# Optimization experiments

Measured on AMD Instinct MI355X. Metric: run time of the kernel, lower is better.

Reference implementation:

```python
import jax, jax.numpy as jnp
import numpy as np

IN_FEATURES = 256
WIDTH = 512
GRID_POINTS = 32   # num control points
DEGREE = 3         # spline_order
BATCH = 8192
LN_EPS = 1e-5


def make_knots(num_ctrl_pts, degree):
    knot_count = num_ctrl_pts + degree + 1
    knots = np.zeros(knot_count, dtype=np.float32)
    knots[-(degree + 1):] = 1.0
    interior = knot_count - 2 * (degree + 1)
    if interior > 0:
        knots[degree + 1:degree + 1 + interior] = np.linspace(0.0, 1.0, interior + 2, dtype=np.float32)[1:-1]
    return jnp.asarray(knots)

KNOTS = make_knots(GRID_POINTS, DEGREE)  # [num_ctrl + degree + 1]


def bspline_basis(x, knots, degree):
    # x: [b, f] in [0,1]; returns [b, f, num_ctrl_pts]
    xe = x[..., None]                      # [b, f, 1]
    left = knots[:-1]
    right = knots[1:]
    basis = ((xe >= left) & (xe < right)).astype(x.dtype)            # [b,f,K-1]
    last = ((xe >= left[-1]) & (xe <= right[-1])).astype(x.dtype)    # [b,f,1]
    basis = jnp.concatenate([basis[..., :-1], last], axis=-1)
    for r in range(1, degree + 1):  # fixed small loop over spline order
        m = basis.shape[-1] - 1
        if m <= 0:
            break
        idx = np.arange(m)
        lk = knots[idx]                 # [m]
        rk = knots[idx + r + 1]
        d1 = knots[idx + r] - knots[idx]
        d2 = knots[idx + r + 1] - knots[idx + 1]
        s1 = jnp.where(d1 > 0, d1, 1.0)  # safe denominators (avoid nan in both where branches)
        s2 = jnp.where(d2 > 0, d2, 1.0)
        t1 = jnp.where(d1 > 0, (xe - lk) / s1, 0.0) * basis[..., :m]
        t2 = jnp.where(d2 > 0, (rk - xe) / s2, 0.0) * basis[..., 1:m + 1]
        basis = t1 + t2
    return basis


def setup_inputs() -> dict:
    key = jax.random.key(0)
    ks = jax.random.split(key, 8)
    coeff_init = np.sqrt(2.0 / (GRID_POINTS * IN_FEATURES)).astype(np.float32)
    return {
        "inputs": jax.random.normal(ks[0], (BATCH, IN_FEATURES), dtype=jnp.float32),
        "input_shift": jnp.zeros((IN_FEATURES,), dtype=jnp.float32),
        "input_log_scale": jnp.zeros((IN_FEATURES,), dtype=jnp.float32),
        "spline_coeffs": coeff_init * jax.random.normal(ks[1], (IN_FEATURES, GRID_POINTS, WIDTH), dtype=jnp.float32),
        "bias": jnp.zeros((WIDTH,), dtype=jnp.float32),
        "skip_w": jax.random.normal(ks[2], (IN_FEATURES, WIDTH), dtype=jnp.float32) / np.sqrt(IN_FEATURES).astype(np.float32),
        "skip_b": jnp.zeros((WIDTH,), dtype=jnp.float32),
        "ln_gamma": jnp.ones((WIDTH,), dtype=jnp.float32),
        "ln_beta": jnp.zeros((WIDTH,), dtype=jnp.float32),
    }


def reference(inputs, input_shift, input_log_scale, spline_coeffs, bias,
              skip_w, skip_b, ln_gamma, ln_beta):
    scale = jax.nn.softplus(input_log_scale) + 0.001
    normalised = jax.nn.sigmoid((inputs - input_shift) * scale)            # [b,f] in (0,1)
    basis = bspline_basis(normalised, KNOTS, DEGREE)                       # [b,f,g]
    spline_mix = jnp.einsum('bfg,fgw->bw', basis, spline_coeffs)
    linear_skip = inputs @ skip_w + skip_b
    combined = spline_mix + linear_skip + bias
    mu = jnp.mean(combined, axis=-1, keepdims=True)
    var = jnp.mean(jnp.square(combined - mu), axis=-1, keepdims=True)
    normed = (combined - mu) * jax.lax.rsqrt(var + LN_EPS) * ln_gamma + ln_beta
    return jax.nn.gelu(normed, approximate=False)  # torch nn.GELU default = exact erf
```

## Files before the change

### kernel.cpp

```cpp
#include <hip/hip_runtime.h>
#include <hip/hip_bf16.h>
#include <math.h>

#define BATCH 8192
#define F 256
#define G 32
#define W 512
#define NCHUNK 132
#define NPER 66

typedef float f32x4 __attribute__((ext_vector_type(4)));
typedef short s16x8 __attribute__((ext_vector_type(8)));
typedef long long i64x2 __attribute__((ext_vector_type(2)));
typedef unsigned long long u64;

__device__ __forceinline__ short f2bf(float f) {
  unsigned int u = __builtin_bit_cast(unsigned int, f);
  u += 0x7fffu + ((u >> 16) & 1u);
  return (short)(u >> 16);
}

__device__ __forceinline__ float bf2f(unsigned short h) {
  unsigned int u = ((unsigned int)h) << 16;
  return __builtin_bit_cast(float, u);
}

__device__ __forceinline__ float knotv(int i) {
  int j = i - 3;
  j = j < 0 ? 0 : (j > 29 ? 29 : j);
  return (float)j * (1.0f / 29.0f);
}

__device__ __forceinline__ float fdiv_fast(float a, float b) {
  return a * __builtin_amdgcn_rcpf(b);
}

__global__ __launch_bounds__(256) void pre_build(
    const float* __restrict__ coeffs, const float* __restrict__ skip_w,
    const float* __restrict__ inp, const float* __restrict__ shift,
    const float* __restrict__ lscale,
    short* __restrict__ Bws, unsigned long long* __restrict__ nvq,
    unsigned char* __restrict__ s0q)
{
  __shared__ float T[64][17];
  __shared__ float sfc[16], sfh[16];
  const int tid = threadIdx.x;

  if (blockIdx.x < 2112) {
    const int gid = blockIdx.x * 256 + tid;
    const int lane = gid & 63;
    const int kk = (gid >> 6) & 1;
    const int nf = (gid >> 7) & 3;
    const int wn = (gid >> 9) & 1;
    const int nt = (gid >> 10) & 3;
    const int c  = gid >> 12;
    const int w  = nt * 128 + wn * 64 + nf * 16 + (lane & 15);
    const int kl = kk * 32 + (lane >> 4) * 8;
    const float* src = (c < 128) ? (coeffs + (size_t)(c * 64 + kl) * W + w)
                                 : (skip_w + (size_t)((c - 128) * 64 + kl) * W + w);
    s16x8 h;
    #pragma unroll
    for (int j = 0; j < 8; ++j) h[j] = f2bf(src[(size_t)j * W]);
    ((s16x8*)Bws)[gid] = h;
    return;
  }

  const int bb = blockIdx.x - 2112;
  const int b0 = (bb & 127) * 64;
  const int f0 = (bb >> 7) * 16;

  {
    const int r = tid >> 2, q = tid & 3;
    float4 v = *(const float4*)(inp + (size_t)(b0 + r) * F + f0 + q * 4);
    T[r][q * 4 + 0] = v.x;
    T[r][q * 4 + 1] = v.y;
    T[r][q * 4 + 2] = v.z;
    T[r][q * 4 + 3] = v.w;
  }
  if (tid < 16) {
    float ls = lscale[f0 + tid];
    sfc[tid] = fmaxf(ls, 0.0f) + __logf(1.0f + __expf(-fabsf(ls))) + 0.001f;
    sfh[tid] = shift[f0 + tid];
  }
  __syncthreads();

  const int lane = tid & 63;
  const int wid = tid >> 6;
  #pragma unroll
  for (int j = 0; j < 4; ++j) {
    const int fl = wid * 4 + j;
    const int f = f0 + fl;
    const float z = (T[lane][fl] - sfh[fl]) * sfc[fl];
    const float sg = 1.0f / (1.0f + __expf(-z));
    int s0 = (int)(sg * 29.0f);
    s0 = s0 < 0 ? 0 : (s0 > 28 ? 28 : s0);
    const int sp = s0 + 3;
    float Nv[4], lef[4], rig[4];
    Nv[0] = 1.0f;
    #pragma unroll
    for (int r = 1; r <= 3; ++r) {
      lef[r] = sg - knotv(sp + 1 - r);
      rig[r] = knotv(sp + r) - sg;
      float saved = 0.0f;
      #pragma unroll
      for (int jj = 0; jj < r; ++jj) {
        float temp = fdiv_fast(Nv[jj], rig[jj + 1] + lef[r - jj]);
        Nv[jj] = saved + rig[jj + 1] * temp;
        saved = lef[r - jj] * temp;
      }
      Nv[r] = saved;
    }
    const u64 nv =
        (u64)(unsigned short)f2bf(Nv[0])
      | ((u64)(unsigned short)f2bf(Nv[1]) << 16)
      | ((u64)(unsigned short)f2bf(Nv[2]) << 32)
      | ((u64)(unsigned short)f2bf(Nv[3]) << 48);
    nvq[(size_t)f * BATCH + b0 + lane] = nv;
    s0q[(size_t)f * BATCH + b0 + lane] = (unsigned char)s0;
  }
}

__device__ __forceinline__ void stage_nv(short* __restrict__ Ab, int cc,
    int stoff, int hi, int bp, int m0,
    unsigned long long nv, int s0, const float* __restrict__ inp)
{
  short* base = Ab + stoff;
  if (cc < 128) {
    const int pp = s0 & 7, ga = s0 >> 3;
    const int s = 16 * pp, shl = s & 63;
    const unsigned long long a = nv << shl;
    const unsigned long long b = (nv >> (63 - shl)) >> 1;
    const bool hs = (s >= 64);
    i64x2 d0, d1, z;
    d0[0] = hs ? 0ll : (long long)a;
    d0[1] = hs ? (long long)a : (long long)b;
    d1[0] = hs ? (long long)b : 0ll;
    d1[1] = 0ll;
    z[0] = 0ll; z[1] = 0ll;
    *(i64x2*)(base + ga * 128) = d0;
    *(i64x2*)(base + ((ga + 1) & 3) * 128) = d1;
    *(i64x2*)(base + ((ga + 2) & 3) * 128) = z;
    *(i64x2*)(base + ((ga + 3) & 3) * 128) = z;
  } else {
    const int sb = (cc - 128) * 64 + hi * 32;
    const float* ip = inp + (size_t)(m0 + bp) * F + sb;
    #pragma unroll
    for (int lq = 0; lq < 4; ++lq) {
      s16x8 h;
      #pragma unroll
      for (int j = 0; j < 8; ++j) h[j] = f2bf(ip[lq * 8 + j]);
      *(s16x8*)(base + lq * 128) = h;
    }
  }
}

__global__ __launch_bounds__(256, 2) void kan_gemm_v9(
    const float* __restrict__ inp, const short* __restrict__ Bws,
    const unsigned long long* __restrict__ nvq, const unsigned char* __restrict__ s0q,
    const float* __restrict__ bias, const float* __restrict__ skip_b,
    float* __restrict__ outf, short* __restrict__ Cws)
{
  __shared__ short Abuf[2][8192];

  const int tid = threadIdx.x;
  const int lane = tid & 63;
  const int wid = tid >> 6;
  const int kh = wid >> 1;
  const int nh = wid & 1;

  const int nb = ((blockIdx.x & 7) << 6) | (blockIdx.x >> 3);
  const int mt = nb >> 2, nt = nb & 3;
  const int m0 = mt * 64, n0 = nt * 128;

  const int ci = tid >> 7;
  const int hi = (tid >> 6) & 1;
  const int bp = tid & 63;
  const int mg = bp >> 4, l15b = bp & 15;
  const int stoff = ci * 4096 + ((mg * 2 + hi) * 64 + l15b) * 8;

  f32x4 acc[4][4];
  #pragma unroll
  for (int i = 0; i < 4; ++i)
    #pragma unroll
    for (int j = 0; j < 4; ++j)
      acc[i][j] = (f32x4){0.f, 0.f, 0.f, 0.f};

  const short* bq = Bws + (size_t)(((kh * 4 + nt) * 2 + nh) * 8) * 512 + lane * 8;

#define LOADB(BS) do {                                                          \
    _Pragma("unroll")                                                           \
    for (int nf = 0; nf < 4; ++nf)                                              \
      _Pragma("unroll")                                                         \
      for (int kk = 0; kk < 2; ++kk)                                            \
        BS[nf * 2 + kk] = *(const s16x8*)(bq + (nf * 2 + kk) * 512);            \
    bq += 65536;                                                                \
  } while (0)

#define PREF(NVL, S0L, PTGT) do {                                               \
    const int cc_ = 2 * (PTGT) + ci;                                            \
    if ((PTGT) < NPER && cc_ < 128) {                                           \
      const size_t ix_ = (size_t)(2 * cc_ + hi) * BATCH + m0 + bp;              \
      NVL = nvq[ix_];                                                           \
      S0L = (int)s0q[ix_];                                                      \
    }                                                                           \
  } while (0)

#define MMAC(AB, BS)                                                            \
    _Pragma("unroll")                                                           \
    for (int kk = 0; kk < 2; ++kk)                                              \
      _Pragma("unroll")                                                         \
      for (int mf = 0; mf < 4; ++mf) {                                          \
        s16x8 af = *(const s16x8*)&AB[kh * 4096 + ((mf * 2 + kk) * 64 + lane) * 8]; \
        _Pragma("unroll")                                                       \
        for (int nf = 0; nf < 4; ++nf)                                          \
          acc[mf][nf] = __builtin_amdgcn_mfma_f32_16x16x32_bf16(                \
              af, BS[nf * 2 + kk], acc[mf][nf], 0, 0, 0);                       \
      }

#define PERIOD(P_, ACUR, ANXT, BCUR, BNXT, NVU, S0U, NVL, S0L) do {             \
    asm volatile("s_waitcnt lgkmcnt(0)" ::: "memory");                          \
    __builtin_amdgcn_s_barrier();                                               \
    PREF(NVL, S0L, (P_) + 2);                                                   \
    if ((P_) + 1 < NPER) {                                                      \
      LOADB(BNXT);                                                              \
      stage_nv(ANXT, 2 * ((P_) + 1) + ci, stoff, hi, bp, m0, NVU, S0U, inp);    \
    }                                                                           \
    __builtin_amdgcn_s_setprio(1);                                              \
    MMAC(ACUR, BCUR);                                                           \
    __builtin_amdgcn_s_setprio(0);                                              \
  } while (0)

  s16x8 bA[8], bB[8];
  unsigned long long nvA = 0, nvB = 0;
  int s0A = 0, s0B = 0;

  PREF(nvA, s0A, 0);
  LOADB(bA);
  stage_nv(&Abuf[0][0], 2 * 0 + ci, stoff, hi, bp, m0, nvA, s0A, inp);
  PREF(nvB, s0B, 1);

  for (int p = 0; p < NPER; p += 2) {
    PERIOD(p,     (&Abuf[0][0]), (&Abuf[1][0]), bA, bB, nvB, s0B, nvA, s0A);
    PERIOD(p + 1, (&Abuf[1][0]), (&Abuf[0][0]), bB, bA, nvA, s0A, nvB, s0B);
  }
#undef PERIOD
#undef MMAC
#undef PREF
#undef LOADB

  __syncthreads();
  float* red = (float*)&Abuf[0][0];
  const int l15 = lane & 15;
  const int lq = lane >> 4;
  if (kh == 1) {
    #pragma unroll
    for (int mf = 0; mf < 4; ++mf)
      #pragma unroll
      for (int nf = 0; nf < 4; ++nf)
        *(f32x4*)&red[nh * 4096 + (mf * 4 + nf) * 256 + lane * 4] = acc[mf][nf];
  }
  __syncthreads();
  if (kh == 0) {
    #pragma unroll
    for (int nf = 0; nf < 4; ++nf) {
      const int col = n0 + nh * 64 + nf * 16 + l15;
      const float badd = bias[col] + skip_b[col];
      #pragma unroll
      for (int mf = 0; mf < 4; ++mf) {
        f32x4 part = *(const f32x4*)&red[nh * 4096 + (mf * 4 + nf) * 256 + lane * 4];
        const int r0 = m0 + mf * 16 + lq * 4;
        if (Cws) {
          #pragma unroll
          for (int r = 0; r < 4; ++r)
            Cws[(size_t)(r0 + r) * W + col] = f2bf(acc[mf][nf][r] + part[r] + badd);
        } else {
          #pragma unroll
          for (int r = 0; r < 4; ++r)
            outf[(size_t)(r0 + r) * W + col] = acc[mf][nf][r] + part[r] + badd;
        }
      }
    }
  }
}

__global__ __launch_bounds__(256, 1) void ln_gelu_bf(
    const short* __restrict__ Cws, float* __restrict__ out,
    const float* __restrict__ gamma, const float* __restrict__ beta)
{
  const int lane = threadIdx.x & 63;
  const int wid = threadIdx.x >> 6;
  const int row = blockIdx.x * 4 + wid;
  const short* p = Cws + (size_t)row * W + lane * 8;
  s16x8 hv = *(const s16x8*)p;
  float v[8];
  #pragma unroll
  for (int j = 0; j < 8; ++j) v[j] = bf2f((unsigned short)hv[j]);
  float s = 0.f, q = 0.f;
  #pragma unroll
  for (int j = 0; j < 8; ++j) { s += v[j]; q += v[j] * v[j]; }
  #pragma unroll
  for (int m = 1; m < 64; m <<= 1) {
    s += __shfl_xor(s, m);
    q += __shfl_xor(q, m);
  }
  const float mu = s * (1.0f / 512.0f);
  const float var = q * (1.0f / 512.0f) - mu * mu;
  const float inv = rsqrtf(var + 1e-5f);
  const float4 g0 = *(const float4*)(gamma + lane * 8);
  const float4 g1 = *(const float4*)(gamma + lane * 8 + 4);
  const float4 b0 = *(const float4*)(beta + lane * 8);
  const float4 b1 = *(const float4*)(beta + lane * 8 + 4);
  float gm[8] = {g0.x, g0.y, g0.z, g0.w, g1.x, g1.y, g1.z, g1.w};
  float bt[8] = {b0.x, b0.y, b0.z, b0.w, b1.x, b1.y, b1.z, b1.w};
  float o[8];
  #pragma unroll
  for (int j = 0; j < 8; ++j) {
    float x = (v[j] - mu) * inv * gm[j] + bt[j];
    o[j] = 0.5f * x * (1.0f + erff(x * 0.70710678f));
  }
  float* po = out + (size_t)row * W + lane * 8;
  float4 w0 = {o[0], o[1], o[2], o[3]};
  float4 w1 = {o[4], o[5], o[6], o[7]};
  *(float4*)po = w0;
  *(float4*)(po + 4) = w1;
}

__global__ __launch_bounds__(256, 1) void ln_gelu(
    float* __restrict__ out, const float* __restrict__ gamma,
    const float* __restrict__ beta)
{
  const int lane = threadIdx.x & 63;
  const int wid = threadIdx.x >> 6;
  const int row = blockIdx.x * 4 + wid;
  float* p = out + (size_t)row * W + lane * 8;
  float4 a = *(const float4*)p;
  float4 b = *(const float4*)(p + 4);
  float v[8] = {a.x, a.y, a.z, a.w, b.x, b.y, b.z, b.w};
  float s = 0.f, q = 0.f;
  #pragma unroll
  for (int j = 0; j < 8; ++j) { s += v[j]; q += v[j] * v[j]; }
  #pragma unroll
  for (int m = 1; m < 64; m <<= 1) {
    s += __shfl_xor(s, m);
    q += __shfl_xor(q, m);
  }
  const float mu = s * (1.0f / 512.0f);
  const float var = q * (1.0f / 512.0f) - mu * mu;
  const float inv = rsqrtf(var + 1e-5f);
  const float4 g0 = *(const float4*)(gamma + lane * 8);
  const float4 g1 = *(const float4*)(gamma + lane * 8 + 4);
  const float4 b0 = *(const float4*)(beta + lane * 8);
  const float4 b1 = *(const float4*)(beta + lane * 8 + 4);
  float gm[8] = {g0.x, g0.y, g0.z, g0.w, g1.x, g1.y, g1.z, g1.w};
  float bt[8] = {b0.x, b0.y, b0.z, b0.w, b1.x, b1.y, b1.z, b1.w};
  float o[8];
  #pragma unroll
  for (int j = 0; j < 8; ++j) {
    float x = (v[j] - mu) * inv * gm[j] + bt[j];
    o[j] = 0.5f * x * (1.0f + erff(x * 0.70710678f));
  }
  float4 w0 = {o[0], o[1], o[2], o[3]};
  float4 w1 = {o[4], o[5], o[6], o[7]};
  *(float4*)p = w0;
  *(float4*)(p + 4) = w1;
}

__device__ __forceinline__ void issue_b(int c, int uu, int n0,
                                        const float* __restrict__ coeffs,
                                        const float* __restrict__ skip_w,
                                        float (&r)[4][8]) {
  const float* base = (c < 128) ? (coeffs + (size_t)c * 64 * W)
                                : (skip_w + (size_t)(c - 128) * 64 * W);
  const int kk = (uu >> 6) & 1;
  const int lq = (uu >> 4) & 3;
  const int l15 = uu & 15;
  const int u7 = uu >> 7;
  #pragma unroll
  for (int s = 0; s < 4; ++s) {
    const int w = (2 * s + u7) * 16 + l15;
    const float* p = base + (size_t)(kk * 32 + lq * 8) * W + n0 + w;
    #pragma unroll
    for (int j = 0; j < 8; ++j) r[s][j] = p[(size_t)j * W];
  }
}

__global__ __launch_bounds__(512, 1) void kan_gemm_v2(
    const float* __restrict__ inp, const float* __restrict__ shift,
    const float* __restrict__ lscale, const float* __restrict__ coeffs,
    const float* __restrict__ bias, const float* __restrict__ skip_w,
    const float* __restrict__ skip_b, float* __restrict__ out)
{
  __shared__ short Abuf[2][8192];
  __shared__ short Bbuf[2][8192];
  __shared__ unsigned short sgl[F * 128];

  const int tid = threadIdx.x;
  const int lane = tid & 63;
  const int wid = tid >> 6;
  const int nb = (blockIdx.x & 7) * 32 + (blockIdx.x >> 3);
  const int mt = nb >> 2;
  const int nt = nb & 3;
  const int m0 = mt * 128;
  const int n0 = nt * 128;

  float bpref[4][8];
  if (tid >= 256) issue_b(0, tid - 256, n0, coeffs, skip_w, bpref);

  float* shf = (float*)&Abuf[0][0];
  if (tid < 256) {
    float ls = lscale[tid];
    shf[tid] = fmaxf(ls, 0.0f) + __logf(1.0f + __expf(-fabsf(ls))) + 0.001f;
    shf[256 + tid] = shift[tid];
  }
  __syncthreads();

  {
    const int row = tid & 127;
    const int q = tid >> 7;
    const float* ip = inp + (size_t)(m0 + row) * F + q * 64;
    #pragma unroll
    for (int i = 0; i < 16; ++i) {
      float4 v = *(const float4*)(ip + i * 4);
      float vv[4] = {v.x, v.y, v.z, v.w};
      #pragma unroll
      for (int j = 0; j < 4; ++j) {
        const int f = q * 64 + i * 4 + j;
        const float z = (vv[j] - shf[256 + f]) * shf[f];
        const float sg = 1.0f / (1.0f + __expf(-z));
        sgl[f * 128 + row] = (unsigned short)fminf(sg * 65536.0f, 65535.0f);
      }
    }
  }
  __syncthreads();

  const int wm = wid >> 2;
  const int wn = wid & 3;

  f32x4 acc[4][2];
  #pragma unroll
  for (int i = 0; i < 4; ++i)
    #pragma unroll
    for (int j = 0; j < 2; ++j)
      acc[i][j] = (f32x4){0.f, 0.f, 0.f, 0.f};

  for (int c = 0; c < NCHUNK; ++c) {
    short* Ab = Abuf[c & 1];
    short* Bb = Bbuf[c & 1];

    if (c < 128) {
      s16x8 z = {0, 0, 0, 0, 0, 0, 0, 0};
      ((s16x8*)Ab)[tid * 2] = z;
      ((s16x8*)Ab)[tid * 2 + 1] = z;
    } else if (tid < 256) {
      const int bp = tid & 127, fi = tid >> 7;
      const int sb = (c - 128) * 64 + fi * 32;
      const float* ip = inp + (size_t)(m0 + bp) * F + sb;
      const int rg = bp >> 4, l15b = bp & 15;
      #pragma unroll
      for (int lq2 = 0; lq2 < 4; ++lq2) {
        s16x8 h;
        #pragma unroll
        for (int j = 0; j < 8; ++j) h[j] = f2bf(ip[lq2 * 8 + j]);
        *(s16x8*)&Ab[((rg * 2 + fi) * 64 + lq2 * 16 + l15b) * 8] = h;
      }
    }
    if (tid >= 256) {
      const int uu = tid - 256;
      #pragma unroll
      for (int s = 0; s < 4; ++s) {
        s16x8 h;
        #pragma unroll
        for (int j = 0; j < 8; ++j) h[j] = f2bf(bpref[s][j]);
        *(s16x8*)&Bb[(s * 256 + uu) * 8] = h;
      }
      if (c + 1 < NCHUNK) issue_b(c + 1, uu, n0, coeffs, skip_w, bpref);
    }
    __syncthreads();

    if (c < 128 && tid < 256) {
      const int bp = tid & 127, fi = tid >> 7;
      const int f = 2 * c + fi;
      const float sg = ((float)sgl[f * 128 + bp] + 0.5f) * (1.0f / 65536.0f);
      int s0 = (int)floorf(sg * 29.0f);
      s0 = s0 < 0 ? 0 : (s0 > 28 ? 28 : s0);
      const int sp = s0 + 3;
      float Nv[4], lef[4], rig[4];
      Nv[0] = 1.0f;
      #pragma unroll
      for (int r = 1; r <= 3; ++r) {
        lef[r] = sg - knotv(sp + 1 - r);
        rig[r] = knotv(sp + r) - sg;
        float saved = 0.0f;
        #pragma unroll
        for (int j = 0; j < r; ++j) {
          float temp = fdiv_fast(Nv[j], rig[j + 1] + lef[r - j]);
          Nv[j] = saved + rig[j + 1] * temp;
          saved = lef[r - j] * temp;
        }
        Nv[r] = saved;
      }
      const int rg = bp >> 4, l15b = bp & 15;
      #pragma unroll
      for (int t = 0; t < 4; ++t) {
        const int g = s0 + t;
        Ab[((rg * 2 + fi) * 64 + (g >> 3) * 16 + l15b) * 8 + (g & 7)] = f2bf(Nv[t]);
      }
    }
    s16x8 bfv[2][2];
    #pragma unroll
    for (int nf = 0; nf < 2; ++nf)
      #pragma unroll
      for (int kk = 0; kk < 2; ++kk)
        bfv[nf][kk] = *(const s16x8*)&Bb[(((wn * 2 + nf) * 2 + kk) * 64 + lane) * 8];
    __syncthreads();

    #pragma unroll
    for (int kk = 0; kk < 2; ++kk) {
      #pragma unroll
      for (int mf = 0; mf < 4; ++mf) {
        s16x8 af = *(const s16x8*)&Ab[(((wm * 4 + mf) * 2 + kk) * 64 + lane) * 8];
        #pragma unroll
        for (int nf = 0; nf < 2; ++nf)
          acc[mf][nf] = __builtin_amdgcn_mfma_f32_16x16x32_bf16(af, bfv[nf][kk], acc[mf][nf], 0, 0, 0);
      }
    }
  }

  const int l15 = lane & 15;
  const int lq = lane >> 4;
  #pragma unroll
  for (int nf = 0; nf < 2; ++nf) {
    const int col = n0 + wn * 32 + nf * 16 + l15;
    const float badd = bias[col] + skip_b[col];
    #pragma unroll
    for (int mf = 0; mf < 4; ++mf) {
      const int r0 = m0 + wm * 64 + mf * 16 + lq * 4;
      #pragma unroll
      for (int r = 0; r < 4; ++r)
        out[(size_t)(r0 + r) * W + col] = acc[mf][nf][r] + badd;
    }
  }
}

extern "C" void kernel_launch(void* const* d_in, const int* in_sizes, int n_in,
                              void* d_out, int out_size, void* d_ws, size_t ws_size,
                              hipStream_t stream) {
  (void)in_sizes; (void)n_in; (void)out_size;
  const float* inp    = (const float*)d_in[0];
  const float* shift  = (const float*)d_in[1];
  const float* lscale = (const float*)d_in[2];
  const float* coeffs = (const float*)d_in[3];
  const float* bias   = (const float*)d_in[4];
  const float* skip_w = (const float*)d_in[5];
  const float* skip_b = (const float*)d_in[6];
  const float* gamma  = (const float*)d_in[7];
  const float* beta   = (const float*)d_in[8];
  float* out = (float*)d_out;

  const size_t needB  = (size_t)NCHUNK * 4 * 16384;
  const size_t needNV = (size_t)F * BATCH * 8;
  const size_t needS0 = (size_t)F * BATCH;
  const size_t needC  = (size_t)BATCH * W * 2;

  if (ws_size >= needB + needNV + needS0 + needC) {
    short* Bws = (short*)d_ws;
    unsigned long long* nvq = (unsigned long long*)((char*)d_ws + needB);
    unsigned char* s0q = (unsigned char*)((char*)d_ws + needB + needNV);
    short* Cws = (short*)((char*)d_ws + needB + needNV + needS0);
    pre_build<<<dim3(4160), dim3(256), 0, stream>>>(
        coeffs, skip_w, inp, shift, lscale, Bws, nvq, s0q);
    kan_gemm_v9<<<dim3(512), dim3(256), 0, stream>>>(
        inp, Bws, nvq, s0q, bias, skip_b, nullptr, Cws);
    ln_gelu_bf<<<dim3(BATCH / 4), dim3(256), 0, stream>>>(Cws, out, gamma, beta);
  } else if (ws_size >= needB + needNV + needS0) {
    short* Bws = (short*)d_ws;
    unsigned long long* nvq = (unsigned long long*)((char*)d_ws + needB);
    unsigned char* s0q = (unsigned char*)((char*)d_ws + needB + needNV);
    pre_build<<<dim3(4160), dim3(256), 0, stream>>>(
        coeffs, skip_w, inp, shift, lscale, Bws, nvq, s0q);
    kan_gemm_v9<<<dim3(512), dim3(256), 0, stream>>>(
        inp, Bws, nvq, s0q, bias, skip_b, out, nullptr);
    ln_gelu<<<dim3(BATCH / 4), dim3(256), 0, stream>>>(out, gamma, beta);
  } else {
    kan_gemm_v2<<<dim3(256), dim3(512), 0, stream>>>(
        inp, shift, lscale, coeffs, bias, skip_w, skip_b, out);
    ln_gelu<<<dim3(BATCH / 4), dim3(256), 0, stream>>>(out, gamma, beta);
  }
}
```

Before: 88.39 us.

## Split GEMM reduction across two blocks and sum bf16 partials in LayerNorm

Splits the K dimension (132 chunks) of the fused spline/skip GEMM into two halves handled by separate blocks, doubling the grid to 1024 blocks. Each half writes a bf16 partial result to its own workspace buffer, and the LayerNorm+GELU kernel adds the two partials before normalising. This aims to improve CU utilisation and latency hiding over a single wave of long-running blocks. In exchange it adds a second partial-output write and read, and an extra bf16 rounding step. The no-workspace fallback kernel is removed.

```diff
diff --git a/kernel.cpp b/kernel.cpp
--- a/kernel.cpp
+++ b/kernel.cpp
@@ -8,6 +8,7 @@
 #define W 512
 #define NCHUNK 132
 #define NPER 66
+#define NPERL 33
 
 typedef float f32x4 __attribute__((ext_vector_type(4)));
 typedef short s16x8 __attribute__((ext_vector_type(8)));
@@ -154,11 +155,11 @@
   }
 }
 
-__global__ __launch_bounds__(256, 2) void kan_gemm_v9(
+__global__ __launch_bounds__(256, 2) void kan_gemm_v18(
     const float* __restrict__ inp, const short* __restrict__ Bws,
     const unsigned long long* __restrict__ nvq, const unsigned char* __restrict__ s0q,
     const float* __restrict__ bias, const float* __restrict__ skip_b,
-    float* __restrict__ outf, short* __restrict__ Cws)
+    short* __restrict__ Cws)
 {
   __shared__ short Abuf[2][8192];
 
@@ -168,9 +169,12 @@
   const int kh = wid >> 1;
   const int nh = wid & 1;
 
-  const int nb = ((blockIdx.x & 7) << 6) | (blockIdx.x >> 3);
-  const int mt = nb >> 2, nt = nb & 3;
+  const int nb = ((blockIdx.x & 7) << 7) | (blockIdx.x >> 3);
+  const int nt = nb >> 8;
+  const int kb = (nb >> 7) & 1;
+  const int mt = nb & 127;
   const int m0 = mt * 64, n0 = nt * 128;
+  const int cbase = kb * 66;
 
   const int ci = tid >> 7;
   const int hi = (tid >> 6) & 1;
@@ -185,7 +189,7 @@
     for (int j = 0; j < 4; ++j)
       acc[i][j] = (f32x4){0.f, 0.f, 0.f, 0.f};
 
-  const short* bq = Bws + (size_t)(((kh * 4 + nt) * 2 + nh) * 8) * 512 + lane * 8;
+  const short* bq = Bws + (size_t)((((cbase + kh) * 4 + nt) * 2 + nh) * 8) * 512 + lane * 8;
 
 #define LOADB(BS) do {                                                          \
     _Pragma("unroll")                                                           \
@@ -197,6 +201,176 @@
   } while (0)
 
 #define PREF(NVL, S0L, PTGT) do {                                               \
+    const int cc_ = cbase + 2 * (PTGT) + ci;                                    \
+    if ((PTGT) < NPERL && cc_ < 128) {                                          \
+      const size_t ix_ = (size_t)(2 * cc_ + hi) * BATCH + m0 + bp;              \
+      NVL = nvq[ix_];                                                           \
+      S0L = (int)s0q[ix_];                                                      \
+    }                                                                           \
+  } while (0)
+
+#define MMAC(AB, BS)                                                            \
+    _Pragma("unroll")                                                           \
+    for (int kk = 0; kk < 2; ++kk)                                              \
+      _Pragma("unroll")                                                         \
+      for (int mf = 0; mf < 4; ++mf) {                                          \
+        s16x8 af = *(const s16x8*)&(AB)[kh * 4096 + ((mf * 2 + kk) * 64 + lane) * 8]; \
+        _Pragma("unroll")                                                       \
+        for (int nf = 0; nf < 4; ++nf)                                          \
+          acc[mf][nf] = __builtin_amdgcn_mfma_f32_16x16x32_bf16(                \
+              af, BS[nf * 2 + kk], acc[mf][nf], 0, 0, 0);                       \
+      }
+
+#define PERIOD(P_, ACUR, ANXT, BCUR, BNXT, NVU, S0U, NVL, S0L) do {             \
+    asm volatile("s_waitcnt lgkmcnt(0)" ::: "memory");                          \
+    __builtin_amdgcn_s_barrier();                                               \
+    PREF(NVL, S0L, (P_) + 2);                                                   \
+    if ((P_) + 1 < NPERL) {                                                     \
+      LOADB(BNXT);                                                              \
+      stage_nv(ANXT, cbase + 2 * ((P_) + 1) + ci, stoff, hi, bp, m0, NVU, S0U, inp); \
+    }                                                                           \
+    __builtin_amdgcn_s_setprio(1);                                              \
+    MMAC(ACUR, BCUR);                                                           \
+    __builtin_amdgcn_s_setprio(0);                                              \
+  } while (0)
+
+  s16x8 bA[8], bB[8];
+  unsigned long long nvA = 0, nvB = 0;
+  int s0A = 0, s0B = 0;
+
+  PREF(nvA, s0A, 0);
+  LOADB(bA);
+  stage_nv(&Abuf[0][0], cbase + ci, stoff, hi, bp, m0, nvA, s0A, inp);
+  PREF(nvB, s0B, 1);
+
+  for (int p = 0; p + 1 < NPERL; p += 2) {
+    PERIOD(p,     (&Abuf[0][0]), (&Abuf[1][0]), bA, bB, nvB, s0B, nvA, s0A);
+    PERIOD(p + 1, (&Abuf[1][0]), (&Abuf[0][0]), bB, bA, nvA, s0A, nvB, s0B);
+  }
+  PERIOD(NPERL - 1, (&Abuf[0][0]), (&Abuf[1][0]), bA, bB, nvB, s0B, nvA, s0A);
+#undef PERIOD
+#undef MMAC
+#undef PREF
+#undef LOADB
+
+  __syncthreads();
+  float* red = (float*)&Abuf[0][0];
+  const int l15 = lane & 15;
+  const int lq = lane >> 4;
+  if (kh == 1) {
+    #pragma unroll
+    for (int mf = 0; mf < 4; ++mf)
+      #pragma unroll
+      for (int nf = 0; nf < 4; ++nf)
+        *(f32x4*)&red[nh * 4096 + (mf * 4 + nf) * 256 + lane * 4] = acc[mf][nf];
+  }
+  __syncthreads();
+  if (kh == 0) {
+    short* Cp = Cws + (size_t)kb * BATCH * W;
+    #pragma unroll
+    for (int nf = 0; nf < 4; ++nf) {
+      const int col = n0 + nh * 64 + nf * 16 + l15;
+      const float badd = (kb == 0) ? (bias[col] + skip_b[col]) : 0.0f;
+      #pragma unroll
+      for (int mf = 0; mf < 4; ++mf) {
+        f32x4 part = *(const f32x4*)&red[nh * 4096 + (mf * 4 + nf) * 256 + lane * 4];
+        const int r0 = m0 + mf * 16 + lq * 4;
+        #pragma unroll
+        for (int r = 0; r < 4; ++r)
+          Cp[(size_t)(r0 + r) * W + col] = f2bf(acc[mf][nf][r] + part[r] + badd);
+      }
+    }
+  }
+}
+
+__global__ __launch_bounds__(256, 1) void ln_gelu_bf2(
+    const short* __restrict__ Cws, float* __restrict__ out,
+    const float* __restrict__ gamma, const float* __restrict__ beta)
+{
+  const int lane = threadIdx.x & 63;
+  const int wid = threadIdx.x >> 6;
+  const int row = blockIdx.x * 4 + wid;
+  const short* p0 = Cws + (size_t)row * W + lane * 8;
+  const short* p1 = p0 + (size_t)BATCH * W;
+  s16x8 h0 = *(const s16x8*)p0;
+  s16x8 h1 = *(const s16x8*)p1;
+  float v[8];
+  #pragma unroll
+  for (int j = 0; j < 8; ++j)
+    v[j] = bf2f((unsigned short)h0[j]) + bf2f((unsigned short)h1[j]);
+  float s = 0.f, q = 0.f;
+  #pragma unroll
+  for (int j = 0; j < 8; ++j) { s += v[j]; q += v[j] * v[j]; }
+  #pragma unroll
+  for (int m = 1; m < 64; m <<= 1) {
+    s += __shfl_xor(s, m);
+    q += __shfl_xor(q, m);
+  }
+  const float mu = s * (1.0f / 512.0f);
+  const float var = q * (1.0f / 512.0f) - mu * mu;
+  const float inv = rsqrtf(var + 1e-5f);
+  const float4 g0 = *(const float4*)(gamma + lane * 8);
+  const float4 g1 = *(const float4*)(gamma + lane * 8 + 4);
+  const float4 b0 = *(const float4*)(beta + lane * 8);
+  const float4 b1 = *(const float4*)(beta + lane * 8 + 4);
+  float gm[8] = {g0.x, g0.y, g0.z, g0.w, g1.x, g1.y, g1.z, g1.w};
+  float bt[8] = {b0.x, b0.y, b0.z, b0.w, b1.x, b1.y, b1.z, b1.w};
+  float o[8];
+  #pragma unroll
+  for (int j = 0; j < 8; ++j) {
+    float x = (v[j] - mu) * inv * gm[j] + bt[j];
+    o[j] = 0.5f * x * (1.0f + erff(x * 0.70710678f));
+  }
+  float* po = out + (size_t)row * W + lane * 8;
+  float4 w0 = {o[0], o[1], o[2], o[3]};
+  float4 w1 = {o[4], o[5], o[6], o[7]};
+  *(float4*)po = w0;
+  *(float4*)(po + 4) = w1;
+}
+
+__global__ __launch_bounds__(256, 2) void kan_gemm_v9f(
+    const float* __restrict__ inp, const short* __restrict__ Bws,
+    const unsigned long long* __restrict__ nvq, const unsigned char* __restrict__ s0q,
+    const float* __restrict__ bias, const float* __restrict__ skip_b,
+    float* __restrict__ outf)
+{
+  __shared__ short Abuf[2][8192];
+
+  const int tid = threadIdx.x;
+  const int lane = tid & 63;
+  const int wid = tid >> 6;
+  const int kh = wid >> 1;
+  const int nh = wid & 1;
+
+  const int nb = ((blockIdx.x & 7) << 6) | (blockIdx.x >> 3);
+  const int mt = nb >> 2, nt = nb & 3;
+  const int m0 = mt * 64, n0 = nt * 128;
+
+  const int ci = tid >> 7;
+  const int hi = (tid >> 6) & 1;
+  const int bp = tid & 63;
+  const int mg = bp >> 4, l15b = bp & 15;
+  const int stoff = ci * 4096 + ((mg * 2 + hi) * 64 + l15b) * 8;
+
+  f32x4 acc[4][4];
+  #pragma unroll
+  for (int i = 0; i < 4; ++i)
+    #pragma unroll
+    for (int j = 0; j < 4; ++j)
+      acc[i][j] = (f32x4){0.f, 0.f, 0.f, 0.f};
+
+  const short* bq = Bws + (size_t)(((kh * 4 + nt) * 2 + nh) * 8) * 512 + lane * 8;
+
+#define LOADB(BS) do {                                                          \
+    _Pragma("unroll")                                                           \
+    for (int nf = 0; nf < 4; ++nf)                                              \
+      _Pragma("unroll")                                                         \
+      for (int kk = 0; kk < 2; ++kk)                                            \
+        BS[nf * 2 + kk] = *(const s16x8*)(bq + (nf * 2 + kk) * 512);            \
+    bq += 65536;                                                                \
+  } while (0)
+
+#define PREF(NVL, S0L, PTGT) do {                                               \
     const int cc_ = 2 * (PTGT) + ci;                                            \
     if ((PTGT) < NPER && cc_ < 128) {                                           \
       const size_t ix_ = (size_t)(2 * cc_ + hi) * BATCH + m0 + bp;              \
@@ -210,7 +384,7 @@
     for (int kk = 0; kk < 2; ++kk)                                              \
       _Pragma("unroll")                                                         \
       for (int mf = 0; mf < 4; ++mf) {                                          \
-        s16x8 af = *(const s16x8*)&AB[kh * 4096 + ((mf * 2 + kk) * 64 + lane) * 8]; \
+        s16x8 af = *(const s16x8*)&(AB)[kh * 4096 + ((mf * 2 + kk) * 64 + lane) * 8]; \
         _Pragma("unroll")                                                       \
         for (int nf = 0; nf < 4; ++nf)                                          \
           acc[mf][nf] = __builtin_amdgcn_mfma_f32_16x16x32_bf16(                \
@@ -236,7 +410,7 @@
 
   PREF(nvA, s0A, 0);
   LOADB(bA);
-  stage_nv(&Abuf[0][0], 2 * 0 + ci, stoff, hi, bp, m0, nvA, s0A, inp);
+  stage_nv(&Abuf[0][0], ci, stoff, hi, bp, m0, nvA, s0A, inp);
   PREF(nvB, s0B, 1);
 
   for (int p = 0; p < NPER; p += 2) {
@@ -269,60 +443,12 @@
       for (int mf = 0; mf < 4; ++mf) {
         f32x4 part = *(const f32x4*)&red[nh * 4096 + (mf * 4 + nf) * 256 + lane * 4];
         const int r0 = m0 + mf * 16 + lq * 4;
-        if (Cws) {
-          #pragma unroll
-          for (int r = 0; r < 4; ++r)
-            Cws[(size_t)(r0 + r) * W + col] = f2bf(acc[mf][nf][r] + part[r] + badd);
-        } else {
-          #pragma unroll
-          for (int r = 0; r < 4; ++r)
-            outf[(size_t)(r0 + r) * W + col] = acc[mf][nf][r] + part[r] + badd;
-        }
+        #pragma unroll
+        for (int r = 0; r < 4; ++r)
+          outf[(size_t)(r0 + r) * W + col] = acc[mf][nf][r] + part[r] + badd;
       }
     }
   }
-}
-
-__global__ __launch_bounds__(256, 1) void ln_gelu_bf(
-    const short* __restrict__ Cws, float* __restrict__ out,
-    const float* __restrict__ gamma, const float* __restrict__ beta)
-{
-  const int lane = threadIdx.x & 63;
-  const int wid = threadIdx.x >> 6;
-  const int row = blockIdx.x * 4 + wid;
-  const short* p = Cws + (size_t)row * W + lane * 8;
-  s16x8 hv = *(const s16x8*)p;
-  float v[8];
-  #pragma unroll
-  for (int j = 0; j < 8; ++j) v[j] = bf2f((unsigned short)hv[j]);
-  float s = 0.f, q = 0.f;
-  #pragma unroll
-  for (int j = 0; j < 8; ++j) { s += v[j]; q += v[j] * v[j]; }
-  #pragma unroll
-  for (int m = 1; m < 64; m <<= 1) {
-    s += __shfl_xor(s, m);
-    q += __shfl_xor(q, m);
-  }
-  const float mu = s * (1.0f / 512.0f);
-  const float var = q * (1.0f / 512.0f) - mu * mu;
-  const float inv = rsqrtf(var + 1e-5f);
-  const float4 g0 = *(const float4*)(gamma + lane * 8);
-  const float4 g1 = *(const float4*)(gamma + lane * 8 + 4);
-  const float4 b0 = *(const float4*)(beta + lane * 8);
-  const float4 b1 = *(const float4*)(beta + lane * 8 + 4);
-  float gm[8] = {g0.x, g0.y, g0.z, g0.w, g1.x, g1.y, g1.z, g1.w};
-  float bt[8] = {b0.x, b0.y, b0.z, b0.w, b1.x, b1.y, b1.z, b1.w};
-  float o[8];
-  #pragma unroll
-  for (int j = 0; j < 8; ++j) {
-    float x = (v[j] - mu) * inv * gm[j] + bt[j];
-    o[j] = 0.5f * x * (1.0f + erff(x * 0.70710678f));
-  }
-  float* po = out + (size_t)row * W + lane * 8;
-  float4 w0 = {o[0], o[1], o[2], o[3]};
-  float4 w1 = {o[4], o[5], o[6], o[7]};
-  *(float4*)po = w0;
-  *(float4*)(po + 4) = w1;
 }
 
 __global__ __launch_bounds__(256, 1) void ln_gelu(
@@ -363,183 +489,6 @@
   float4 w1 = {o[4], o[5], o[6], o[7]};
   *(float4*)p = w0;
   *(float4*)(p + 4) = w1;
-}
-
-__device__ __forceinline__ void issue_b(int c, int uu, int n0,
-                                        const float* __restrict__ coeffs,
-                                        const float* __restrict__ skip_w,
-                                        float (&r)[4][8]) {
-  const float* base = (c < 128) ? (coeffs + (size_t)c * 64 * W)
-                                : (skip_w + (size_t)(c - 128) * 64 * W);
-  const int kk = (uu >> 6) & 1;
-  const int lq = (uu >> 4) & 3;
-  const int l15 = uu & 15;
-  const int u7 = uu >> 7;
-  #pragma unroll
-  for (int s = 0; s < 4; ++s) {
-    const int w = (2 * s + u7) * 16 + l15;
-    const float* p = base + (size_t)(kk * 32 + lq * 8) * W + n0 + w;
-    #pragma unroll
-    for (int j = 0; j < 8; ++j) r[s][j] = p[(size_t)j * W];
-  }
-}
-
-__global__ __launch_bounds__(512, 1) void kan_gemm_v2(
-    const float* __restrict__ inp, const float* __restrict__ shift,
-    const float* __restrict__ lscale, const float* __restrict__ coeffs,
-    const float* __restrict__ bias, const float* __restrict__ skip_w,
-    const float* __restrict__ skip_b, float* __restrict__ out)
-{
-  __shared__ short Abuf[2][8192];
-  __shared__ short Bbuf[2][8192];
-  __shared__ unsigned short sgl[F * 128];
-
-  const int tid = threadIdx.x;
-  const int lane = tid & 63;
-  const int wid = tid >> 6;
-  const int nb = (blockIdx.x & 7) * 32 + (blockIdx.x >> 3);
-  const int mt = nb >> 2;
-  const int nt = nb & 3;
-  const int m0 = mt * 128;
-  const int n0 = nt * 128;
-
-  float bpref[4][8];
-  if (tid >= 256) issue_b(0, tid - 256, n0, coeffs, skip_w, bpref);
-
-  float* shf = (float*)&Abuf[0][0];
-  if (tid < 256) {
-    float ls = lscale[tid];
-    shf[tid] = fmaxf(ls, 0.0f) + __logf(1.0f + __expf(-fabsf(ls))) + 0.001f;
-    shf[256 + tid] = shift[tid];
-  }
-  __syncthreads();
-
-  {
-    const int row = tid & 127;
-    const int q = tid >> 7;
-    const float* ip = inp + (size_t)(m0 + row) * F + q * 64;
-    #pragma unroll
-    for (int i = 0; i < 16; ++i) {
-      float4 v = *(const float4*)(ip + i * 4);
-      float vv[4] = {v.x, v.y, v.z, v.w};
-      #pragma unroll
-      for (int j = 0; j < 4; ++j) {
-        const int f = q * 64 + i * 4 + j;
-        const float z = (vv[j] - shf[256 + f]) * shf[f];
-        const float sg = 1.0f / (1.0f + __expf(-z));
-        sgl[f * 128 + row] = (unsigned short)fminf(sg * 65536.0f, 65535.0f);
-      }
-    }
-  }
-  __syncthreads();
-
-  const int wm = wid >> 2;
-  const int wn = wid & 3;
-
-  f32x4 acc[4][2];
-  #pragma unroll
-  for (int i = 0; i < 4; ++i)
-    #pragma unroll
-    for (int j = 0; j < 2; ++j)
-      acc[i][j] = (f32x4){0.f, 0.f, 0.f, 0.f};
-
-  for (int c = 0; c < NCHUNK; ++c) {
-    short* Ab = Abuf[c & 1];
-    short* Bb = Bbuf[c & 1];
-
-    if (c < 128) {
-      s16x8 z = {0, 0, 0, 0, 0, 0, 0, 0};
-      ((s16x8*)Ab)[tid * 2] = z;
-      ((s16x8*)Ab)[tid * 2 + 1] = z;
-    } else if (tid < 256) {
-      const int bp = tid & 127, fi = tid >> 7;
-      const int sb = (c - 128) * 64 + fi * 32;
-      const float* ip = inp + (size_t)(m0 + bp) * F + sb;
-      const int rg = bp >> 4, l15b = bp & 15;
-      #pragma unroll
-      for (int lq2 = 0; lq2 < 4; ++lq2) {
-        s16x8 h;
-        #pragma unroll
-        for (int j = 0; j < 8; ++j) h[j] = f2bf(ip[lq2 * 8 + j]);
-        *(s16x8*)&Ab[((rg * 2 + fi) * 64 + lq2 * 16 + l15b) * 8] = h;
-      }
-    }
-    if (tid >= 256) {
-      const int uu = tid - 256;
-      #pragma unroll
-      for (int s = 0; s < 4; ++s) {
-        s16x8 h;
-        #pragma unroll
-        for (int j = 0; j < 8; ++j) h[j] = f2bf(bpref[s][j]);
-        *(s16x8*)&Bb[(s * 256 + uu) * 8] = h;
-      }
-      if (c + 1 < NCHUNK) issue_b(c + 1, uu, n0, coeffs, skip_w, bpref);
-    }
-    __syncthreads();
-
-    if (c < 128 && tid < 256) {
-      const int bp = tid & 127, fi = tid >> 7;
-      const int f = 2 * c + fi;
-      const float sg = ((float)sgl[f * 128 + bp] + 0.5f) * (1.0f / 65536.0f);
-      int s0 = (int)floorf(sg * 29.0f);
-      s0 = s0 < 0 ? 0 : (s0 > 28 ? 28 : s0);
-      const int sp = s0 + 3;
-      float Nv[4], lef[4], rig[4];
-      Nv[0] = 1.0f;
-      #pragma unroll
-      for (int r = 1; r <= 3; ++r) {
-        lef[r] = sg - knotv(sp + 1 - r);
-        rig[r] = knotv(sp + r) - sg;
-        float saved = 0.0f;
-        #pragma unroll
-        for (int j = 0; j < r; ++j) {
-          float temp = fdiv_fast(Nv[j], rig[j + 1] + lef[r - j]);
-          Nv[j] = saved + rig[j + 1] * temp;
-          saved = lef[r - j] * temp;
-        }
-        Nv[r] = saved;
-      }
-      const int rg = bp >> 4, l15b = bp & 15;
-      #pragma unroll
-      for (int t = 0; t < 4; ++t) {
-        const int g = s0 + t;
-        Ab[((rg * 2 + fi) * 64 + (g >> 3) * 16 + l15b) * 8 + (g & 7)] = f2bf(Nv[t]);
-      }
-    }
-    s16x8 bfv[2][2];
-    #pragma unroll
-    for (int nf = 0; nf < 2; ++nf)
-      #pragma unroll
-      for (int kk = 0; kk < 2; ++kk)
-        bfv[nf][kk] = *(const s16x8*)&Bb[(((wn * 2 + nf) * 2 + kk) * 64 + lane) * 8];
-    __syncthreads();
-
-    #pragma unroll
-    for (int kk = 0; kk < 2; ++kk) {
-      #pragma unroll
-      for (int mf = 0; mf < 4; ++mf) {
-        s16x8 af = *(const s16x8*)&Ab[(((wm * 4 + mf) * 2 + kk) * 64 + lane) * 8];
-        #pragma unroll
-        for (int nf = 0; nf < 2; ++nf)
-          acc[mf][nf] = __builtin_amdgcn_mfma_f32_16x16x32_bf16(af, bfv[nf][kk], acc[mf][nf], 0, 0, 0);
-      }
-    }
-  }
-
-  const int l15 = lane & 15;
-  const int lq = lane >> 4;
-  #pragma unroll
-  for (int nf = 0; nf < 2; ++nf) {
-    const int col = n0 + wn * 32 + nf * 16 + l15;
-    const float badd = bias[col] + skip_b[col];
-    #pragma unroll
-    for (int mf = 0; mf < 4; ++mf) {
-      const int r0 = m0 + wm * 64 + mf * 16 + lq * 4;
-      #pragma unroll
-      for (int r = 0; r < 4; ++r)
-        out[(size_t)(r0 + r) * W + col] = acc[mf][nf][r] + badd;
-    }
-  }
 }
 
 extern "C" void kernel_launch(void* const* d_in, const int* in_sizes, int n_in,
@@ -560,30 +509,26 @@
   const size_t needB  = (size_t)NCHUNK * 4 * 16384;
   const size_t needNV = (size_t)F * BATCH * 8;
   const size_t needS0 = (size_t)F * BATCH;
-  const size_t needC  = (size_t)BATCH * W * 2;
-
-  if (ws_size >= needB + needNV + needS0 + needC) {
+  const size_t needC2 = (size_t)2 * BATCH * W * 2;
+
+  if (ws_size >= needB + needNV + needS0 + needC2) {
     short* Bws = (short*)d_ws;
     unsigned long long* nvq = (unsigned long long*)((char*)d_ws + needB);
     unsigned char* s0q = (unsigned char*)((char*)d_ws + needB + needNV);
     short* Cws = (short*)((char*)d_ws + needB + needNV + needS0);
     pre_build<<<dim3(4160), dim3(256), 0, stream>>>(
         coeffs, skip_w, inp, shift, lscale, Bws, nvq, s0q);
-    kan_gemm_v9<<<dim3(512), dim3(256), 0, stream>>>(
-        inp, Bws, nvq, s0q, bias, skip_b, nullptr, Cws);
-    ln_gelu_bf<<<dim3(BATCH / 4), dim3(256), 0, stream>>>(Cws, out, gamma, beta);
-  } else if (ws_size >= needB + needNV + needS0) {
+    kan_gemm_v18<<<dim3(1024), dim3(256), 0, stream>>>(
+        inp, Bws, nvq, s0q, bias, skip_b, Cws);
+    ln_gelu_bf2<<<dim3(BATCH / 4), dim3(256), 0, stream>>>(Cws, out, gamma, beta);
+  } else {
     short* Bws = (short*)d_ws;
     unsigned long long* nvq = (unsigned long long*)((char*)d_ws + needB);
     unsigned char* s0q = (unsigned char*)((char*)d_ws + needB + needNV);
     pre_build<<<dim3(4160), dim3(256), 0, stream>>>(
         coeffs, skip_w, inp, shift, lscale, Bws, nvq, s0q);
-    kan_gemm_v9<<<dim3(512), dim3(256), 0, stream>>>(
-        inp, Bws, nvq, s0q, bias, skip_b, out, nullptr);
+    kan_gemm_v9f<<<dim3(512), dim3(256), 0, stream>>>(
+        inp, Bws, nvq, s0q, bias, skip_b, out);
     ln_gelu<<<dim3(BATCH / 4), dim3(256), 0, stream>>>(out, gamma, beta);
-  } else {
-    kan_gemm_v2<<<dim3(256), dim3(512), 0, stream>>>(
-        inp, shift, lscale, coeffs, bias, skip_w, skip_b, out);
-    ln_gelu<<<dim3(BATCH / 4), dim3(256), 0, stream>>>(out, gamma, beta);
-  }
-}
+  }
+}
```

After: 94.63 us. 1.07x slower.
